# Kernel optimization log

Hardware: AMD Instinct MI355X
Metric: run time of the kernel (lower is better)

The kernel has to match this reference:

```python
import jax, jax.numpy as jnp
import numpy as np

H = 4096      # num_patches (sequence length)
WS = 8        # window_size
SHIFT = 4     # shift_size
NH = 8        # num_heads
DIM = 512     # embedding dim
HD = DIM // NH
NW = H // WS  # windows per batch element
B = 16
LN_EPS = 1e-5


def _layer_norm(x, g, b):
    m = jnp.mean(x, axis=-1, keepdims=True)
    v = jnp.var(x, axis=-1, keepdims=True)
    return (x - m) * jax.lax.rsqrt(v + LN_EPS) * g + b


def _window_partition(x):
    # Faithful to the repo: reshape->permute(nW<->ws)->flatten, giving strided windows.
    Bx, N, C = x.shape
    return x.reshape(Bx, N // WS, WS, C).transpose(0, 2, 1, 3).reshape(-1, WS, C)


def _window_reverse(w, N, Bx):
    C = w.shape[-1]
    return w.reshape(Bx, N // WS, WS, C).transpose(0, 2, 1, 3).reshape(Bx, N, C)


def _attn_mask():
    # Built exactly as in __init__ (numpy, constant at trace time): (NW, WS, WS)
    m = np.zeros((1, H, 1), np.float32)
    m[:, :H - WS] = 0.0
    m[:, H - WS:H - SHIFT] = 1.0
    m[:, H - SHIFT:] = 2.0
    mw = m.reshape(1, NW, WS, 1).transpose(0, 2, 1, 3).reshape(-1, WS)  # (NW, WS)
    d = mw[:, None, :] - mw[:, :, None]
    return np.where(d != 0, np.float32(-100.0), np.float32(0.0))


def _forward(x, norm1_g, norm1_b, qkv_w, qkv_b, proj_w, proj_b,
             norm2_g, norm2_b, fc1_w, fc1_b, fc2_w, fc2_b):
    Bx = x.shape[0]
    shortcut = x
    xn = _layer_norm(x, norm1_g, norm1_b)
    xs = jnp.roll(xn, -SHIFT, axis=1)
    xw = _window_partition(xs)                       # (Bx*NW, WS, DIM)
    B_ = xw.shape[0]
    qkv = xw @ qkv_w.T + qkv_b                       # (B_, WS, 3*DIM)
    qkv = qkv.reshape(B_, WS, 3, NH, HD).transpose(2, 0, 3, 1, 4)
    q, k, v = qkv[0], qkv[1], qkv[2]                 # (B_, NH, WS, HD)
    attn = jnp.einsum('bhqd,bhkd->bhqk', q, k) * (HD ** -0.5)
    mask = jnp.asarray(_attn_mask())                 # (NW, WS, WS)
    attn = attn.reshape(B_ // NW, NW, NH, WS, WS) + mask[None, :, None]
    attn = jax.nn.softmax(attn.reshape(B_, NH, WS, WS), axis=-1)
    o = jnp.einsum('bhqk,bhkd->bqhd', attn, v).reshape(B_, WS, DIM)
    o = o @ proj_w.T + proj_b
    xr = _window_reverse(o, H, Bx)
    xr = jnp.roll(xr, SHIFT, axis=1)
    x1 = shortcut + xr
    h = _layer_norm(x1, norm2_g, norm2_b)
    h = jax.nn.gelu(h @ fc1_w.T + fc1_b, approximate=False)
    h = h @ fc2_w.T + fc2_b
    return x1 + h


def setup_inputs() -> dict:
    key = jax.random.key(0)
    ks = jax.random.split(key, 8)
    s = 0.02
    return {
        'x': jax.random.normal(ks[0], (B, H, DIM), jnp.float32),
        'norm1_g': jnp.ones((DIM,), jnp.float32),
        'norm1_b': jnp.zeros((DIM,), jnp.float32),
        'qkv_w': jax.random.normal(ks[1], (3 * DIM, DIM), jnp.float32) * s,
        'qkv_b': jnp.zeros((3 * DIM,), jnp.float32),
        'proj_w': jax.random.normal(ks[2], (DIM, DIM), jnp.float32) * s,
        'proj_b': jnp.zeros((DIM,), jnp.float32),
        'norm2_g': jnp.ones((DIM,), jnp.float32),
        'norm2_b': jnp.zeros((DIM,), jnp.float32),
        'fc1_w': jax.random.normal(ks[3], (4 * DIM, DIM), jnp.float32) * s,
        'fc1_b': jnp.zeros((4 * DIM,), jnp.float32),
        'fc2_w': jax.random.normal(ks[4], (DIM, 4 * DIM), jnp.float32) * s,
        'fc2_b': jnp.zeros((DIM,), jnp.float32),
    }


def reference(x, norm1_g, norm1_b, qkv_w, qkv_b, proj_w, proj_b,
              norm2_g, norm2_b, fc1_w, fc1_b, fc2_w, fc2_b):
    return _forward(x, norm1_g, norm1_b, qkv_w, qkv_b, proj_w, proj_b,
                    norm2_g, norm2_b, fc1_w, fc1_b, fc2_w, fc2_b)
```

## Files before the change

### kernel.cpp

```cpp
#include <hip/hip_runtime.h>
#include <hip/hip_bf16.h>
#include <math.h>

typedef unsigned short ushortT;
typedef __attribute__((ext_vector_type(8))) short short8;
typedef __attribute__((ext_vector_type(4))) short short4v;
typedef __attribute__((ext_vector_type(4))) float f32x4;
typedef __attribute__((ext_vector_type(4))) float float4v;

#define TOK 65536
#define NSEQ 4096
#define DIM 512

__device__ __forceinline__ float bf2f(ushortT u) {
  union { float f; unsigned int i; } v; v.i = ((unsigned int)u) << 16; return v.f;
}
__device__ __forceinline__ ushortT f2bf(float f) {
  union { float f; unsigned int i; } v; v.f = f;
  unsigned int r = v.i + 0x7fffu + ((v.i >> 16) & 1u);
  return (ushortT)(r >> 16);
}

__device__ __forceinline__ float fast_gelu(float x) {
  const float y = fabsf(x) * 0.70710678118654752f;
  const float t = __builtin_amdgcn_rcpf(__builtin_fmaf(0.3275911f, y, 1.f));
  float p = 1.061405429f;
  p = __builtin_fmaf(p, t, -1.453152027f);
  p = __builtin_fmaf(p, t, 1.421413741f);
  p = __builtin_fmaf(p, t, -0.284496736f);
  p = __builtin_fmaf(p, t, 0.254829592f);
  p = p * t;
  const float e = __builtin_amdgcn_exp2f(-y * y * 1.4426950408889634f);
  float erfv = __builtin_fmaf(-p, e, 1.f);
  erfv = copysignf(erfv, x);
  return 0.5f * x * (1.f + erfv);
}

#define GLOAD_LDS(gp, lp) __builtin_amdgcn_global_load_lds( \
    (const __attribute__((address_space(1))) unsigned int*)(gp), \
    (__attribute__((address_space(3))) unsigned int*)(lp), 16, 0, 0)

#define BAR __builtin_amdgcn_s_barrier()
#define VMC(n) asm volatile("s_waitcnt vmcnt(" #n ")" ::: "memory")
#define SB0 __builtin_amdgcn_sched_barrier(0)

__global__ void cvt_kernel(const float* __restrict__ in, ushortT* __restrict__ out, int n4) {
  int i = blockIdx.x * 256 + threadIdx.x;
  if (i >= n4) return;
  float4v v = *(const float4v*)(in + (size_t)i * 4);
  short4v o;
#pragma unroll
  for (int j = 0; j < 4; ++j) o[j] = (short)f2bf(v[j]);
  *(short4v*)(out + (size_t)i * 4) = o;
}

template <bool INBF>
__global__ __launch_bounds__(256)
void ln_kernel(const void* __restrict__ inp, const float* __restrict__ gw,
               const float* __restrict__ bw, ushortT* __restrict__ out)
{
  const int lane = threadIdx.x & 63;
  const size_t tok = (size_t)blockIdx.x * 4 + (threadIdx.x >> 6);
  const int col = lane * 8;
  float x[8];
  if constexpr (INBF) {
    short8 v = *(const short8*)((const ushortT*)inp + tok * DIM + col);
#pragma unroll
    for (int j = 0; j < 8; ++j) x[j] = bf2f((ushortT)v[j]);
  } else {
    const float* p = (const float*)inp + tok * DIM + col;
    float4v a = *(const float4v*)p, b = *(const float4v*)(p + 4);
#pragma unroll
    for (int j = 0; j < 4; ++j) { x[j] = a[j]; x[4 + j] = b[j]; }
  }
  float s = 0.f, ss = 0.f;
#pragma unroll
  for (int j = 0; j < 8; ++j) { s += x[j]; ss += x[j] * x[j]; }
#pragma unroll
  for (int off = 1; off < 64; off <<= 1) {
    s += __shfl_xor(s, off, 64);
    ss += __shfl_xor(ss, off, 64);
  }
  const float mean = s * (1.f / 512.f);
  const float var = ss * (1.f / 512.f) - mean * mean;
  const float rstd = rsqrtf(var + 1e-5f);
  float4v g1 = *(const float4v*)(gw + col), g2 = *(const float4v*)(gw + col + 4);
  float4v b1 = *(const float4v*)(bw + col), b2 = *(const float4v*)(bw + col + 4);
  short8 o;
#pragma unroll
  for (int j = 0; j < 4; ++j) {
    o[j]     = (short)f2bf((x[j]     - mean) * rstd * g1[j] + b1[j]);
    o[4 + j] = (short)f2bf((x[4 + j] - mean) * rstd * g2[j] + b2[j]);
  }
  *(short8*)(out + tok * DIM + col) = o;
}

#define STG(bA, bB, kt) do { \
    const ushortT* _ga = gA + (size_t)(kt) * 32; \
    const ushortT* _gb = gB + (size_t)(kt) * 32; \
    GLOAD_LDS(_ga,                  (bA) + w * 1024); \
    GLOAD_LDS(_ga + (size_t)16 * K, (bA) + w * 1024 + 512); \
    GLOAD_LDS(_gb,                  (bB) + w * 1024); \
    GLOAD_LDS(_gb + (size_t)16 * K, (bB) + w * 1024 + 512); \
  } while (0)

template <int EPI>
__global__ __launch_bounds__(512, 2)
void gemm256(const ushortT* __restrict__ A, const ushortT* __restrict__ Bt,
             const float* __restrict__ bias, int M, int N, int K,
             ushortT* __restrict__ outb, float* __restrict__ outf,
             const float* __restrict__ resf, const ushortT* __restrict__ resb)
{
  __shared__ __align__(16) ushortT sm[65536];

  const int tid = threadIdx.x;
  const int w = tid >> 6, l = tid & 63;
  const int wr = w >> 2, wc = w & 3;

  const int nwg = gridDim.x * gridDim.y;
  int wg = blockIdx.y * gridDim.x + blockIdx.x;
  {
    const int q = nwg >> 3, r8 = nwg & 7;
    const int xc = wg & 7, yc = wg >> 3;
    wg = (xc < r8 ? xc * (q + 1) : r8 * (q + 1) + (xc - r8) * q) + yc;
  }
  const int nbn = N >> 8;
  const int mb = wg / nbn, nb = wg % nbn;
  const int m0 = mb << 8, n0 = nb << 8;
  const int NT = K >> 5;

  const int scw = ((l & 3) ^ ((l >> 2) & 3) ^ (l >> 4)) << 3;
  const ushortT* gA = A  + (size_t)(m0 + w * 32 + (l >> 2)) * K + scw;
  const ushortT* gB = Bt + (size_t)(n0 + w * 32 + (l >> 2)) * K + scw;

  const int rl = l & 15, ql = l >> 4;
  const int xr = (rl & 3) ^ ((rl >> 2) & 3);
  const int aoff = (wr * 128 + rl) * 32 + ((ql ^ xr) << 3);
  const int boff = (wc * 64 + rl) * 32 + ((ql ^ xr) << 3);

  f32x4 acc[8][4];
  const f32x4 zero = {0.f, 0.f, 0.f, 0.f};
#pragma unroll
  for (int i = 0; i < 8; ++i)
#pragma unroll
    for (int j = 0; j < 4; ++j) acc[i][j] = zero;

  ushortT* a0 = sm;              ushortT* b0 = sm + 8192;
  ushortT* a1 = sm + 16384;      ushortT* b1 = sm + 24576;
  ushortT* a2 = sm + 32768;      ushortT* b2 = sm + 40960;
  ushortT* a3 = sm + 49152;      ushortT* b3 = sm + 57344;

  STG(a0, b0, 0);
  STG(a1, b1, 1);
  STG(a2, b2, 2);
  VMC(8);
  BAR; SB0;

  short8 Af[8], Bf[4];

  for (int t = 0; t < NT; ++t) {
    if (t + 3 < NT) STG(a3, b3, t + 3);
#pragma unroll
    for (int m = 0; m < 8; ++m) Af[m] = *(const short8*)(a0 + aoff + m * 512);
#pragma unroll
    for (int n = 0; n < 4; ++n) Bf[n] = *(const short8*)(b0 + boff + n * 512);
#pragma unroll
    for (int m = 0; m < 8; ++m)
#pragma unroll
      for (int n = 0; n < 4; ++n)
        acc[m][n] = __builtin_amdgcn_mfma_f32_16x16x32_bf16(Af[m], Bf[n], acc[m][n], 0, 0, 0);
    SB0;
    if (t + 4 <= NT)      { VMC(8); }
    else if (t + 3 == NT) { VMC(4); }
    else if (t + 2 == NT) { VMC(0); }
    BAR; SB0;
    ushortT* tp;
    tp = a0; a0 = a1; a1 = a2; a2 = a3; a3 = tp;
    tp = b0; b0 = b1; b1 = b2; b2 = b3; b3 = tp;
  }

  float* const ep = (float*)sm;
#pragma unroll
  for (int p = 0; p < 2; ++p) {
    if (p) BAR;
    if (wr == p) {
#pragma unroll
      for (int m = 0; m < 8; ++m) {
#pragma unroll
        for (int n = 0; n < 4; ++n) {
          const int c = wc * 64 + n * 16 + rl;
          const int pc = c ^ (c >> 3);
          *(f32x4*)(ep + (m * 4 + ql) * 1024 + pc * 4) = acc[m][n];
        }
      }
    }
    BAR;
#pragma unroll
    for (int k = 0; k < 4; ++k) {
      const int rb = w + k * 8;
      const int rowb = 16 * (rb >> 2) + 4 * (rb & 3);
      f32x4 rv[4];
#pragma unroll
      for (int j = 0; j < 4; ++j) {
        const int c = 4 * l + j;
        const int pc = c ^ (c >> 3);
        rv[j] = *(const f32x4*)(ep + rb * 1024 + pc * 4);
      }
      const int col = n0 + 4 * l;
      const float4v bb = *(const float4v*)(bias + col);
#pragma unroll
      for (int i = 0; i < 4; ++i) {
        const size_t row = (size_t)(m0 + p * 128 + rowb + i);
        float v0 = rv[0][i] + bb[0], v1 = rv[1][i] + bb[1],
              v2 = rv[2][i] + bb[2], v3 = rv[3][i] + bb[3];
        if constexpr (EPI == 1) {
          const float4v rr = *(const float4v*)(resf + row * (size_t)N + col);
          v0 += rr[0]; v1 += rr[1]; v2 += rr[2]; v3 += rr[3];
        }
        if constexpr (EPI == 2) {
          v0 = fast_gelu(v0); v1 = fast_gelu(v1); v2 = fast_gelu(v2); v3 = fast_gelu(v3);
        }
        if constexpr (EPI == 3) {
          const short4v rb4 = *(const short4v*)(resb + row * (size_t)N + col);
          v0 += bf2f((ushortT)rb4[0]); v1 += bf2f((ushortT)rb4[1]);
          v2 += bf2f((ushortT)rb4[2]); v3 += bf2f((ushortT)rb4[3]);
          float4v o = {v0, v1, v2, v3};
          *(float4v*)(outf + row * (size_t)N + col) = o;
        } else {
          short4v o;
          o[0] = (short)f2bf(v0); o[1] = (short)f2bf(v1);
          o[2] = (short)f2bf(v2); o[3] = (short)f2bf(v3);
          *(short4v*)(outb + row * (size_t)N + col) = o;
        }
      }
    }
  }
}

__global__ __launch_bounds__(512)
void attn_kernel(const ushortT* __restrict__ qkv, ushortT* __restrict__ out)
{
  __shared__ __align__(16) ushortT sq[8][1544];
  const int wb = blockIdx.x;
  const int b  = wb >> 9;
  const int rr = wb & 511;
  const int w1 = rr >> 6;
  const int g  = rr & 63;
  const int tid = threadIdx.x;

#pragma unroll
  for (int c = 0; c < 3; ++c) {
    const int f = c * 512 + tid;
    const int i = f / 192;
    const int col = (f % 192) * 8;
    const int tin = (64 * g + 8 * i + w1 + 4) & (NSEQ - 1);
    const ushortT* src = qkv + ((size_t)b * NSEQ + tin) * 1536 + col;
    *(short8*)(&sq[i][col]) = *(const short8*)src;
  }
  __syncthreads();

  const int wave = tid >> 6, lane = tid & 63;
  const int h = wave;
  const int qi = lane >> 3, kj = lane & 7;

  float s = 0.f;
  const ushortT* qrow = &sq[qi][h * 64];
  const ushortT* krow = &sq[kj][512 + h * 64];
#pragma unroll
  for (int c = 0; c < 8; ++c) {
    short8 qa = *(const short8*)(qrow + c * 8);
    short8 ka = *(const short8*)(krow + c * 8);
#pragma unroll
    for (int j = 0; j < 8; ++j) s += bf2f((ushortT)qa[j]) * bf2f((ushortT)ka[j]);
  }
  s *= 0.125f;

  const int pq = 64 * g + 8 * qi + w1;
  const int pk = 64 * g + 8 * kj + w1;
  const int cq = (pq < 4088) ? 0 : (pq < 4092 ? 1 : 2);
  const int ck = (pk < 4088) ? 0 : (pk < 4092 ? 1 : 2);
  if (cq != ck) s -= 100.f;

  float mx = s;
  mx = fmaxf(mx, __shfl_xor(mx, 1, 64));
  mx = fmaxf(mx, __shfl_xor(mx, 2, 64));
  mx = fmaxf(mx, __shfl_xor(mx, 4, 64));
  const float e = expf(s - mx);
  float sum = e;
  sum += __shfl_xor(sum, 1, 64);
  sum += __shfl_xor(sum, 2, 64);
  sum += __shfl_xor(sum, 4, 64);
  const float p = e / sum;

  const int dc = lane & 7;
  float o[8];
#pragma unroll
  for (int j = 0; j < 8; ++j) o[j] = 0.f;
#pragma unroll
  for (int k2 = 0; k2 < 8; ++k2) {
    const float pk2 = __shfl(p, (lane & ~7) + k2, 64);
    short8 va = *(const short8*)(&sq[k2][1024 + h * 64 + dc * 8]);
#pragma unroll
    for (int j = 0; j < 8; ++j) o[j] += pk2 * bf2f((ushortT)va[j]);
  }

  const int tout = (512 * qi + 64 * w1 + g + 4) & (NSEQ - 1);
  short8 ov;
#pragma unroll
  for (int j = 0; j < 8; ++j) ov[j] = (short)f2bf(o[j]);
  *(short8*)(out + ((size_t)b * NSEQ + tout) * DIM + h * 64 + dc * 8) = ov;
}

extern "C" void kernel_launch(void* const* d_in, const int* in_sizes, int n_in,
                              void* d_out, int out_size, void* d_ws, size_t ws_size,
                              hipStream_t stream) {
  const float* x      = (const float*)d_in[0];
  const float* n1g    = (const float*)d_in[1];
  const float* n1b    = (const float*)d_in[2];
  const float* qkv_w  = (const float*)d_in[3];
  const float* qkv_b  = (const float*)d_in[4];
  const float* proj_w = (const float*)d_in[5];
  const float* proj_b = (const float*)d_in[6];
  const float* n2g    = (const float*)d_in[7];
  const float* n2b    = (const float*)d_in[8];
  const float* fc1_w  = (const float*)d_in[9];
  const float* fc1_b  = (const float*)d_in[10];
  const float* fc2_w  = (const float*)d_in[11];
  const float* fc2_b  = (const float*)d_in[12];
  float* out = (float*)d_out;

  size_t off = 0;
  char* ws = (char*)d_ws;
  auto alloc = [&](size_t b) { void* p = ws + off; off += (b + 255) & ~(size_t)255; return p; };

  ushortT* qkvw_b = (ushortT*)alloc((size_t)1536 * 512 * 2);
  ushortT* projw_b = (ushortT*)alloc((size_t)512 * 512 * 2);
  ushortT* fc1w_b = (ushortT*)alloc((size_t)2048 * 512 * 2);
  ushortT* fc2w_b = (ushortT*)alloc((size_t)512 * 2048 * 2);
  ushortT* bufA = (ushortT*)alloc((size_t)TOK * 512 * 2);
  ushortT* bufQ = (ushortT*)alloc((size_t)TOK * 1536 * 2);
  ushortT* x1 = bufQ;

  int nch = 1;
  while (nch < 16) {
    size_t need = (size_t)(TOK / nch) * 2048 * 2;
    if (off + need <= ws_size) break;
    nch <<= 1;
  }
  ushortT* h1 = (ushortT*)(ws + off);

  cvt_kernel<<<(1536 * 512 / 4 + 255) / 256, 256, 0, stream>>>(qkv_w, qkvw_b, 1536 * 512 / 4);
  cvt_kernel<<<(512 * 512 / 4 + 255) / 256, 256, 0, stream>>>(proj_w, projw_b, 512 * 512 / 4);
  cvt_kernel<<<(2048 * 512 / 4 + 255) / 256, 256, 0, stream>>>(fc1_w, fc1w_b, 2048 * 512 / 4);
  cvt_kernel<<<(512 * 2048 / 4 + 255) / 256, 256, 0, stream>>>(fc2_w, fc2w_b, 512 * 2048 / 4);

  ln_kernel<false><<<TOK / 4, 256, 0, stream>>>(x, n1g, n1b, bufA);

  gemm256<0><<<dim3(TOK / 256, 1536 / 256), 512, 0, stream>>>(
      bufA, qkvw_b, qkv_b, TOK, 1536, 512, bufQ, nullptr, nullptr, nullptr);

  attn_kernel<<<8192, 512, 0, stream>>>(bufQ, bufA);

  gemm256<1><<<dim3(TOK / 256, 512 / 256), 512, 0, stream>>>(
      bufA, projw_b, proj_b, TOK, 512, 512, x1, nullptr, x, nullptr);

  ln_kernel<true><<<TOK / 4, 256, 0, stream>>>(x1, n2g, n2b, bufA);

  const int tc = TOK / nch;
  for (int c = 0; c < nch; ++c) {
    const ushortT* hin = bufA + (size_t)c * tc * 512;
    gemm256<2><<<dim3(tc / 256, 2048 / 256), 512, 0, stream>>>(
        hin, fc1w_b, fc1_b, tc, 2048, 512, h1, nullptr, nullptr, nullptr);
    gemm256<3><<<dim3(tc / 256, 512 / 256), 512, 0, stream>>>(
        h1, fc2w_b, fc2_b, tc, 512, 2048, nullptr, out + (size_t)c * tc * 512,
        nullptr, x1 + (size_t)c * tc * 512);
  }
}
```

Baseline: 716.0 us.

## Restructure GEMM main loop into double-buffered 64-wide K steps with split staging

Replaces the 4-stage ring of 32-wide K tiles with two 64-wide K buffers, each staged in two halves, so each loop iteration runs two MFMA blocks with interleaved global-to-LDS loads. It changes the LDS swizzle pattern for both writes and reads, and raises wave priority around the MFMA blocks with s_setprio. The aim is to halve loop overhead and barriers per K and to overlap loads with compute better. The cost is less prefetch depth (one tile ahead instead of three) and a new swizzle that must stay consistent.

```diff
diff --git a/kernel.cpp b/kernel.cpp
--- a/kernel.cpp
+++ b/kernel.cpp
@@ -95,13 +95,11 @@
   *(short8*)(out + tok * DIM + col) = o;
 }
 
-#define STG(bA, bB, kt) do { \
-    const ushortT* _ga = gA + (size_t)(kt) * 32; \
-    const ushortT* _gb = gB + (size_t)(kt) * 32; \
-    GLOAD_LDS(_ga,                  (bA) + w * 1024); \
-    GLOAD_LDS(_ga + (size_t)16 * K, (bA) + w * 1024 + 512); \
-    GLOAD_LDS(_gb,                  (bB) + w * 1024); \
-    GLOAD_LDS(_gb + (size_t)16 * K, (bB) + w * 1024 + 512); \
+#define STAGE_HALF(dA, dB, kofs) do { \
+    GLOAD_LDS(gA + (kofs),                (ushortT*)sm + (dA) + w * 1024); \
+    GLOAD_LDS(gA + (kofs) + (size_t)16*K, (ushortT*)sm + (dA) + w * 1024 + 512); \
+    GLOAD_LDS(gB + (kofs),                (ushortT*)sm + (dB) + w * 1024); \
+    GLOAD_LDS(gB + (kofs) + (size_t)16*K, (ushortT*)sm + (dB) + w * 1024 + 512); \
   } while (0)
 
 template <int EPI>
@@ -127,16 +125,16 @@
   const int nbn = N >> 8;
   const int mb = wg / nbn, nb = wg % nbn;
   const int m0 = mb << 8, n0 = nb << 8;
-  const int NT = K >> 5;
-
-  const int scw = ((l & 3) ^ ((l >> 2) & 3) ^ (l >> 4)) << 3;
-  const ushortT* gA = A  + (size_t)(m0 + w * 32 + (l >> 2)) * K + scw;
-  const ushortT* gB = Bt + (size_t)(n0 + w * 32 + (l >> 2)) * K + scw;
+  const int NT = K >> 6;
+
+  const int schunk = ((l & 3) ^ ((l >> 3) & 3)) << 3;
+  const ushortT* gA = A  + (size_t)(m0 + w * 32 + (l >> 2)) * K + schunk;
+  const ushortT* gB = Bt + (size_t)(n0 + w * 32 + (l >> 2)) * K + schunk;
 
   const int rl = l & 15, ql = l >> 4;
-  const int xr = (rl & 3) ^ ((rl >> 2) & 3);
-  const int aoff = (wr * 128 + rl) * 32 + ((ql ^ xr) << 3);
-  const int boff = (wc * 64 + rl) * 32 + ((ql ^ xr) << 3);
+  const int rdsw = (ql ^ ((rl >> 1) & 3)) << 3;
+  const int aoff = (wr * 128 + rl) * 32 + rdsw;
+  const int boff = (wc * 64 + rl) * 32 + rdsw;
 
   f32x4 acc[8][4];
   const f32x4 zero = {0.f, 0.f, 0.f, 0.f};
@@ -145,38 +143,50 @@
 #pragma unroll
     for (int j = 0; j < 4; ++j) acc[i][j] = zero;
 
-  ushortT* a0 = sm;              ushortT* b0 = sm + 8192;
-  ushortT* a1 = sm + 16384;      ushortT* b1 = sm + 24576;
-  ushortT* a2 = sm + 32768;      ushortT* b2 = sm + 40960;
-  ushortT* a3 = sm + 49152;      ushortT* b3 = sm + 57344;
-
-  STG(a0, b0, 0);
-  STG(a1, b1, 1);
-  STG(a2, b2, 2);
-  VMC(8);
-  BAR; SB0;
+  STAGE_HALF(0 * 8192, 32768 + 0 * 8192, 0);
+  STAGE_HALF(1 * 8192, 32768 + 1 * 8192, 32);
+  VMC(4);
+  BAR;
 
   short8 Af[8], Bf[4];
 
   for (int t = 0; t < NT; ++t) {
-    if (t + 3 < NT) STG(a3, b3, t + 3);
-#pragma unroll
-    for (int m = 0; m < 8; ++m) Af[m] = *(const short8*)(a0 + aoff + m * 512);
-#pragma unroll
-    for (int n = 0; n < 4; ++n) Bf[n] = *(const short8*)(b0 + boff + n * 512);
+    const int s0 = (t & 1) << 1;
+    const int ns0 = ((t + 1) & 1) << 1;
+    const ushortT* sA0 = sm + s0 * 8192;
+    const ushortT* sB0 = sm + 32768 + s0 * 8192;
+    const size_t kb = (size_t)(t + 1) * 64;
+
+    if (t + 1 < NT) STAGE_HALF(ns0 * 8192, 32768 + ns0 * 8192, kb);
+#pragma unroll
+    for (int m = 0; m < 8; ++m) Af[m] = *(const short8*)(sA0 + aoff + m * 512);
+#pragma unroll
+    for (int n = 0; n < 4; ++n) Bf[n] = *(const short8*)(sB0 + boff + n * 512);
+    __builtin_amdgcn_s_setprio(1);
 #pragma unroll
     for (int m = 0; m < 8; ++m)
 #pragma unroll
       for (int n = 0; n < 4; ++n)
         acc[m][n] = __builtin_amdgcn_mfma_f32_16x16x32_bf16(Af[m], Bf[n], acc[m][n], 0, 0, 0);
+    __builtin_amdgcn_s_setprio(0);
+    if (t + 1 < NT) STAGE_HALF((ns0 + 1) * 8192, 32768 + (ns0 + 1) * 8192, kb + 32);
     SB0;
-    if (t + 4 <= NT)      { VMC(8); }
-    else if (t + 3 == NT) { VMC(4); }
-    else if (t + 2 == NT) { VMC(0); }
-    BAR; SB0;
-    ushortT* tp;
-    tp = a0; a0 = a1; a1 = a2; a2 = a3; a3 = tp;
-    tp = b0; b0 = b1; b1 = b2; b2 = b3; b3 = tp;
+    if (t + 1 < NT) { VMC(8); } else { VMC(0); }
+    BAR;
+#pragma unroll
+    for (int m = 0; m < 8; ++m) Af[m] = *(const short8*)(sA0 + 8192 + aoff + m * 512);
+#pragma unroll
+    for (int n = 0; n < 4; ++n) Bf[n] = *(const short8*)(sB0 + 8192 + boff + n * 512);
+    __builtin_amdgcn_s_setprio(1);
+#pragma unroll
+    for (int m = 0; m < 8; ++m)
+#pragma unroll
+      for (int n = 0; n < 4; ++n)
+        acc[m][n] = __builtin_amdgcn_mfma_f32_16x16x32_bf16(Af[m], Bf[n], acc[m][n], 0, 0, 0);
+    __builtin_amdgcn_s_setprio(0);
+    SB0;
+    if (t + 1 < NT) { VMC(4); }
+    BAR;
   }
 
   float* const ep = (float*)sm;
```

Result: no change. 706.5 us (-1.3%).

## Shrink GEMM tile to 128x256 with double-buffered LDS and higher occupancy

Applied to the files above, without the earlier changes.

The GEMM block tile drops from 256x256 with a 4-stage LDS pipeline to 128x256 with a 2-stage double buffer, using a smaller LDS footprint and a new swizzle. Launch bounds ask for 4 blocks per CU instead of 2, and the grid doubles in the M dimension. The goal is to raise occupancy and cut per-block LDS and register pressure so wave-level parallelism hides latency. In exchange, each k-step does less MFMA work per byte loaded, and the shallower prefetch waits on vmcnt(0) every iteration.

```diff
diff --git a/kernel.cpp b/kernel.cpp
--- a/kernel.cpp
+++ b/kernel.cpp
@@ -95,23 +95,14 @@
   *(short8*)(out + tok * DIM + col) = o;
 }
 
-#define STG(bA, bB, kt) do { \
-    const ushortT* _ga = gA + (size_t)(kt) * 32; \
-    const ushortT* _gb = gB + (size_t)(kt) * 32; \
-    GLOAD_LDS(_ga,                  (bA) + w * 1024); \
-    GLOAD_LDS(_ga + (size_t)16 * K, (bA) + w * 1024 + 512); \
-    GLOAD_LDS(_gb,                  (bB) + w * 1024); \
-    GLOAD_LDS(_gb + (size_t)16 * K, (bB) + w * 1024 + 512); \
-  } while (0)
-
 template <int EPI>
-__global__ __launch_bounds__(512, 2)
-void gemm256(const ushortT* __restrict__ A, const ushortT* __restrict__ Bt,
+__global__ __launch_bounds__(512, 4)
+void gemm128(const ushortT* __restrict__ A, const ushortT* __restrict__ Bt,
              const float* __restrict__ bias, int M, int N, int K,
              ushortT* __restrict__ outb, float* __restrict__ outf,
              const float* __restrict__ resf, const ushortT* __restrict__ resb)
 {
-  __shared__ __align__(16) ushortT sm[65536];
+  __shared__ __align__(16) ushortT sm[24576];
 
   const int tid = threadIdx.x;
   const int w = tid >> 6, l = tid & 63;
@@ -126,112 +117,109 @@
   }
   const int nbn = N >> 8;
   const int mb = wg / nbn, nb = wg % nbn;
-  const int m0 = mb << 8, n0 = nb << 8;
+  const int m0 = mb << 7, n0 = nb << 8;
   const int NT = K >> 5;
 
-  const int scw = ((l & 3) ^ ((l >> 2) & 3) ^ (l >> 4)) << 3;
-  const ushortT* gA = A  + (size_t)(m0 + w * 32 + (l >> 2)) * K + scw;
-  const ushortT* gB = Bt + (size_t)(n0 + w * 32 + (l >> 2)) * K + scw;
+  const int schunk = ((l & 3) ^ ((l >> 3) & 3)) << 3;
+  const ushortT* gA = A  + (size_t)(m0 + w * 16 + (l >> 2)) * K + schunk;
+  const ushortT* gB = Bt + (size_t)(n0 + w * 16 + (l >> 2)) * K + schunk;
 
   const int rl = l & 15, ql = l >> 4;
-  const int xr = (rl & 3) ^ ((rl >> 2) & 3);
-  const int aoff = (wr * 128 + rl) * 32 + ((ql ^ xr) << 3);
-  const int boff = (wc * 64 + rl) * 32 + ((ql ^ xr) << 3);
-
-  f32x4 acc[8][4];
+  const int q2 = (ql ^ ((rl >> 1) & 3)) << 3;
+  const int aoff = (wr * 64 + rl) * 32 + q2;
+  const int boff = (wc * 64 + rl) * 32 + q2;
+
+  f32x4 acc[4][4];
   const f32x4 zero = {0.f, 0.f, 0.f, 0.f};
 #pragma unroll
-  for (int i = 0; i < 8; ++i)
+  for (int i = 0; i < 4; ++i)
 #pragma unroll
     for (int j = 0; j < 4; ++j) acc[i][j] = zero;
 
-  ushortT* a0 = sm;              ushortT* b0 = sm + 8192;
-  ushortT* a1 = sm + 16384;      ushortT* b1 = sm + 24576;
-  ushortT* a2 = sm + 32768;      ushortT* b2 = sm + 40960;
-  ushortT* a3 = sm + 49152;      ushortT* b3 = sm + 57344;
-
-  STG(a0, b0, 0);
-  STG(a1, b1, 1);
-  STG(a2, b2, 2);
-  VMC(8);
-  BAR; SB0;
-
-  short8 Af[8], Bf[4];
+  int cur = 0;
+  GLOAD_LDS(gA, sm + w * 512);
+  GLOAD_LDS(gB, sm + 8192 + w * 512);
+  GLOAD_LDS(gB + (size_t)128 * K, sm + 8192 + 4096 + w * 512);
+  VMC(0);
+  BAR;
+
+  short8 Af[4], Bf[4];
 
   for (int t = 0; t < NT; ++t) {
-    if (t + 3 < NT) STG(a3, b3, t + 3);
-#pragma unroll
-    for (int m = 0; m < 8; ++m) Af[m] = *(const short8*)(a0 + aoff + m * 512);
-#pragma unroll
-    for (int n = 0; n < 4; ++n) Bf[n] = *(const short8*)(b0 + boff + n * 512);
-#pragma unroll
-    for (int m = 0; m < 8; ++m)
+    const ushortT* Ac = sm + (cur ? 4096 : 0);
+    const ushortT* Bc = sm + 8192 + (cur ? 8192 : 0);
+    if (t + 1 < NT) {
+      const size_t kb = (size_t)(t + 1) * 32;
+      ushortT* An = sm + (cur ? 0 : 4096);
+      ushortT* Bn = sm + 8192 + (cur ? 0 : 8192);
+      GLOAD_LDS(gA + kb, An + w * 512);
+      GLOAD_LDS(gB + kb, Bn + w * 512);
+      GLOAD_LDS(gB + (size_t)128 * K + kb, Bn + 4096 + w * 512);
+    }
+#pragma unroll
+    for (int m = 0; m < 4; ++m) Af[m] = *(const short8*)(Ac + aoff + m * 512);
+#pragma unroll
+    for (int n = 0; n < 4; ++n) Bf[n] = *(const short8*)(Bc + boff + n * 512);
+#pragma unroll
+    for (int m = 0; m < 4; ++m)
 #pragma unroll
       for (int n = 0; n < 4; ++n)
         acc[m][n] = __builtin_amdgcn_mfma_f32_16x16x32_bf16(Af[m], Bf[n], acc[m][n], 0, 0, 0);
     SB0;
-    if (t + 4 <= NT)      { VMC(8); }
-    else if (t + 3 == NT) { VMC(4); }
-    else if (t + 2 == NT) { VMC(0); }
-    BAR; SB0;
-    ushortT* tp;
-    tp = a0; a0 = a1; a1 = a2; a2 = a3; a3 = tp;
-    tp = b0; b0 = b1; b1 = b2; b2 = b3; b3 = tp;
+    if (t + 1 < NT) VMC(0);
+    BAR;
+    cur ^= 1;
   }
 
   float* const ep = (float*)sm;
 #pragma unroll
-  for (int p = 0; p < 2; ++p) {
+  for (int p = 0; p < 4; ++p) {
     if (p) BAR;
-    if (wr == p) {
-#pragma unroll
-      for (int m = 0; m < 8; ++m) {
+    if (wr == (p >> 1)) {
+#pragma unroll
+      for (int mm = 0; mm < 2; ++mm) {
+        const int m = 2 * (p & 1) + mm;
 #pragma unroll
         for (int n = 0; n < 4; ++n) {
           const int c = wc * 64 + n * 16 + rl;
           const int pc = c ^ (c >> 3);
-          *(f32x4*)(ep + (m * 4 + ql) * 1024 + pc * 4) = acc[m][n];
+          *(f32x4*)(ep + (mm * 4 + ql) * 1024 + pc * 4) = acc[m][n];
         }
       }
     }
     BAR;
-#pragma unroll
-    for (int k = 0; k < 4; ++k) {
-      const int rb = w + k * 8;
-      const int rowb = 16 * (rb >> 2) + 4 * (rb & 3);
-      f32x4 rv[4];
-#pragma unroll
-      for (int j = 0; j < 4; ++j) {
-        const int c = 4 * l + j;
-        const int pc = c ^ (c >> 3);
-        rv[j] = *(const f32x4*)(ep + rb * 1024 + pc * 4);
+    f32x4 rv[4];
+#pragma unroll
+    for (int j = 0; j < 4; ++j) {
+      const int c = 4 * l + j;
+      const int pc = c ^ (c >> 3);
+      rv[j] = *(const f32x4*)(ep + w * 1024 + pc * 4);
+    }
+    const int col = n0 + 4 * l;
+    const float4v bb = *(const float4v*)(bias + col);
+#pragma unroll
+    for (int i = 0; i < 4; ++i) {
+      const size_t row = (size_t)(m0 + p * 32 + (w >> 2) * 16 + (w & 3) * 4 + i);
+      float v0 = rv[0][i] + bb[0], v1 = rv[1][i] + bb[1],
+            v2 = rv[2][i] + bb[2], v3 = rv[3][i] + bb[3];
+      if constexpr (EPI == 1) {
+        const float4v rr = *(const float4v*)(resf + row * (size_t)N + col);
+        v0 += rr[0]; v1 += rr[1]; v2 += rr[2]; v3 += rr[3];
       }
-      const int col = n0 + 4 * l;
-      const float4v bb = *(const float4v*)(bias + col);
-#pragma unroll
-      for (int i = 0; i < 4; ++i) {
-        const size_t row = (size_t)(m0 + p * 128 + rowb + i);
-        float v0 = rv[0][i] + bb[0], v1 = rv[1][i] + bb[1],
-              v2 = rv[2][i] + bb[2], v3 = rv[3][i] + bb[3];
-        if constexpr (EPI == 1) {
-          const float4v rr = *(const float4v*)(resf + row * (size_t)N + col);
-          v0 += rr[0]; v1 += rr[1]; v2 += rr[2]; v3 += rr[3];
-        }
-        if constexpr (EPI == 2) {
-          v0 = fast_gelu(v0); v1 = fast_gelu(v1); v2 = fast_gelu(v2); v3 = fast_gelu(v3);
-        }
-        if constexpr (EPI == 3) {
-          const short4v rb4 = *(const short4v*)(resb + row * (size_t)N + col);
-          v0 += bf2f((ushortT)rb4[0]); v1 += bf2f((ushortT)rb4[1]);
-          v2 += bf2f((ushortT)rb4[2]); v3 += bf2f((ushortT)rb4[3]);
-          float4v o = {v0, v1, v2, v3};
-          *(float4v*)(outf + row * (size_t)N + col) = o;
-        } else {
-          short4v o;
-          o[0] = (short)f2bf(v0); o[1] = (short)f2bf(v1);
-          o[2] = (short)f2bf(v2); o[3] = (short)f2bf(v3);
-          *(short4v*)(outb + row * (size_t)N + col) = o;
-        }
+      if constexpr (EPI == 2) {
+        v0 = fast_gelu(v0); v1 = fast_gelu(v1); v2 = fast_gelu(v2); v3 = fast_gelu(v3);
+      }
+      if constexpr (EPI == 3) {
+        const short4v rb4 = *(const short4v*)(resb + row * (size_t)N + col);
+        v0 += bf2f((ushortT)rb4[0]); v1 += bf2f((ushortT)rb4[1]);
+        v2 += bf2f((ushortT)rb4[2]); v3 += bf2f((ushortT)rb4[3]);
+        float4v o = {v0, v1, v2, v3};
+        *(float4v*)(outf + row * (size_t)N + col) = o;
+      } else {
+        short4v o;
+        o[0] = (short)f2bf(v0); o[1] = (short)f2bf(v1);
+        o[2] = (short)f2bf(v2); o[3] = (short)f2bf(v3);
+        *(short4v*)(outb + row * (size_t)N + col) = o;
       }
     }
   }
@@ -356,12 +344,12 @@
 
   ln_kernel<false><<<TOK / 4, 256, 0, stream>>>(x, n1g, n1b, bufA);
 
-  gemm256<0><<<dim3(TOK / 256, 1536 / 256), 512, 0, stream>>>(
+  gemm128<0><<<dim3(TOK / 128, 1536 / 256), 512, 0, stream>>>(
       bufA, qkvw_b, qkv_b, TOK, 1536, 512, bufQ, nullptr, nullptr, nullptr);
 
   attn_kernel<<<8192, 512, 0, stream>>>(bufQ, bufA);
 
-  gemm256<1><<<dim3(TOK / 256, 512 / 256), 512, 0, stream>>>(
+  gemm128<1><<<dim3(TOK / 128, 512 / 256), 512, 0, stream>>>(
       bufA, projw_b, proj_b, TOK, 512, 512, x1, nullptr, x, nullptr);
 
   ln_kernel<true><<<TOK / 4, 256, 0, stream>>>(x1, n2g, n2b, bufA);
@@ -369,9 +357,9 @@
   const int tc = TOK / nch;
   for (int c = 0; c < nch; ++c) {
     const ushortT* hin = bufA + (size_t)c * tc * 512;
-    gemm256<2><<<dim3(tc / 256, 2048 / 256), 512, 0, stream>>>(
+    gemm128<2><<<dim3(tc / 128, 2048 / 256), 512, 0, stream>>>(
         hin, fc1w_b, fc1_b, tc, 2048, 512, h1, nullptr, nullptr, nullptr);
-    gemm256<3><<<dim3(tc / 256, 512 / 256), 512, 0, stream>>>(
+    gemm128<3><<<dim3(tc / 128, 512 / 256), 512, 0, stream>>>(
         h1, fc2w_b, fc2_b, tc, 512, 2048, nullptr, out + (size_t)c * tc * 512,
         nullptr, x1 + (size_t)c * tc * 512);
   }
```

Result: no change. 704.6 us (-1.6%).
